# Kernel optimization log

Measured on AMD Instinct MI355X. Metric: run time of the kernel, lower is better.

Reference implementation:

```python
import jax, jax.numpy as jnp
import numpy as np

C = 256        # channels per FPN level (in_channels == representation_size)
PATCH = 5      # GNN kernel_size == stride
NEG_SLOPE = 0.2
K = 7          # node_connectivities[0]


def _conv1x1(x, w, b):
    return jnp.einsum('bchw,oc->bohw', x, w) + b[None, :, None, None]


def _conv3x3(x, w, b):
    y = jax.lax.conv_general_dilated(x, w, (1, 1), 'SAME',
                                     dimension_numbers=('NCHW', 'OIHW', 'NCHW'))
    return y + b[None, :, None, None]


def _nearest(x, hout, wout):
    hin, win = x.shape[-2:]
    ih = (jnp.arange(hout) * hin) // hout
    iw = (jnp.arange(wout) * win) // wout
    return x[..., ih, :][..., iw]


def _topk_edges(score, k, n):
    # torch: A.scatter(1, topk_idx, topk_val); edge = nonzero(triu(A)); edge=[col,row]
    vals, idx = jax.lax.top_k(score, k)          # per-row top-k
    row = jnp.repeat(jnp.arange(n), k)
    col = idx.reshape(-1)
    val = vals.reshape(-1)
    # triu keeps col>=row; GATv2Conv removes self loops then re-adds one per node
    mask = (col > row) & (val != 0.0)
    loop = jnp.arange(n)
    src = jnp.concatenate([col, loop])           # PyG edge_index[0] = source
    dst = jnp.concatenate([row, loop])
    emask = jnp.concatenate([mask, jnp.ones((n,), bool)])
    return src, dst, emask


def _gatv2(x, src, dst, emask, wl, bl, wr, br, att, bias, n):
    heads, dout = att.shape
    xl = (x @ wl + bl).reshape(n, heads, dout)   # source transform (lin_l)
    xr = (x @ wr + br).reshape(n, heads, dout)   # target transform (lin_r)
    m = xl[src] + xr[dst]                        # [E, H, D]
    e = jnp.sum(jax.nn.leaky_relu(m, NEG_SLOPE) * att[None], axis=-1)  # [E, H]
    e = jnp.where(emask[:, None], e, -1e30)
    emax = jax.ops.segment_max(e, dst, num_segments=n)
    w = jnp.exp(e - emax[dst]) * emask[:, None]
    denom = jax.ops.segment_sum(w, dst, num_segments=n)
    alpha = w / (denom[dst] + 1e-16)
    out = jax.ops.segment_sum(alpha[..., None] * xl[src], dst, num_segments=n)
    return out.reshape(n, heads * dout) + bias


def _gnn(x, p, k):
    # x: [1, C, H, W], H,W divisible by PATCH
    _, c, hh, ww = x.shape
    nh, nw = hh // PATCH, ww // PATCH
    n = nh * nw
    patches = x[0].reshape(c, nh, PATCH, nw, PATCH).transpose(1, 3, 0, 2, 4)
    patches = patches.reshape(n, c, PATCH, PATCH)
    emb = jax.nn.relu(jnp.einsum('ncij,ocij->no', patches, p['conv1_w']) + p['conv1_b'])
    emb = jax.nn.relu(emb @ p['fc2_w'].T + p['fc2_b'])
    # feature-similarity kNN graph
    src, dst, em = _topk_edges(emb @ emb.T, k, n)
    h = jax.nn.elu(_gatv2(emb, src, dst, em, *p['g1'], n))
    h = jax.nn.elu(_gatv2(h, src, dst, em, *p['g2'], n))
    # spatial kNN graph (k smallest distances; self distance 0 drops out via val!=0)
    ii, jj = jnp.meshgrid(jnp.arange(nh) * PATCH, jnp.arange(nw) * PATCH, indexing='ij')
    centers = jnp.stack([ii.reshape(-1), jj.reshape(-1)], -1).astype(x.dtype)
    dist = jnp.sqrt(jnp.sum((centers[:, None] - centers[None]) ** 2, -1))
    src2, dst2, em2 = _topk_edges(-dist, k, n)
    h2 = jax.nn.elu(_gatv2(emb, src2, dst2, em2, *p['g3'], n))
    h2 = jax.nn.elu(_gatv2(h2, src2, dst2, em2, *p['g4'], n))
    hc = jax.nn.relu(jnp.concatenate([h, h2], 1) @ p['fc3_w'].T + p['fc3_b']) + h2
    # torch: reshape(dim,dim,C).swapdims(-1,0) -> [C, nw, nh]
    grid = jnp.transpose(hc.reshape(nh, nw, c), (2, 1, 0))
    # ConvTranspose2d(C, C, 5, stride=5): non-overlapping tiling
    up = jnp.einsum('cij,coab->oiajb', grid, p['convT_w'])
    up = up.reshape(c, nw * PATCH, nh * PATCH) + p['convT_b'][:, None, None]
    return jax.nn.relu(up)[None]


def _forward(feat0, feat1, inner_w, inner_b, layer_w, layer_b, convT_w, convT_b,
             conv1_w, conv1_b, fc2_w, fc2_b, fc3_w, fc3_b,
             g1_wl, g1_bl, g1_wr, g1_br, g1_att, g1_bias,
             g2_wl, g2_bl, g2_wr, g2_br, g2_att, g2_bias,
             g3_wl, g3_bl, g3_wr, g3_br, g3_att, g3_bias,
             g4_wl, g4_bl, g4_wr, g4_br, g4_att, g4_bias, k):
    feats = [feat0, feat1]
    xs = []
    for i, f in enumerate(feats):
        p = dict(conv1_w=conv1_w[i], conv1_b=conv1_b[i],
                 fc2_w=fc2_w[i], fc2_b=fc2_b[i],
                 fc3_w=fc3_w[i], fc3_b=fc3_b[i],
                 convT_w=convT_w[i], convT_b=convT_b[i],
                 g1=(g1_wl[i], g1_bl[i], g1_wr[i], g1_br[i], g1_att[i], g1_bias[i]),
                 g2=(g2_wl[i], g2_bl[i], g2_wr[i], g2_br[i], g2_att[i], g2_bias[i]),
                 g3=(g3_wl[i], g3_bl[i], g3_wr[i], g3_br[i], g3_att[i], g3_bias[i]),
                 g4=(g4_wl[i], g4_bl[i], g4_wr[i], g4_br[i], g4_att[i], g4_bias[i]))
        xs.append(f + _gnn(f, p, k))
    # top-down FPN
    last = _conv1x1(xs[1], inner_w[1], inner_b[1])
    out1 = _conv3x3(last, layer_w[1], layer_b[1])
    inner0 = _conv1x1(xs[0], inner_w[0], inner_b[0])
    td = _nearest(last, xs[0].shape[-2], xs[0].shape[-1])
    out0 = _conv3x3(inner0 + td, layer_w[0], layer_b[0])
    return out0, out1


def setup_inputs() -> dict:
    key = jax.random.key(0)
    keys = jax.random.split(key, 48)
    it = iter(range(48))
    def rn(shape, s=0.05):
        return (jax.random.normal(keys[next(it)], shape) * s).astype(jnp.float32)
    H8 = 8 * C
    inp = dict(
        feat0=rn((1, C, 200, 200), 1.0),
        feat1=rn((1, C, 100, 100), 1.0),
        inner_w=rn((2, C, C)), inner_b=rn((2, C)),
        layer_w=rn((2, C, C, 3, 3)), layer_b=rn((2, C)),
        convT_w=rn((2, C, C, PATCH, PATCH)), convT_b=rn((2, C)),
        conv1_w=rn((2, C, C, PATCH, PATCH)), conv1_b=rn((2, C)),
        fc2_w=rn((2, C, C)), fc2_b=rn((2, C)),
        fc3_w=rn((2, C, 2 * C)), fc3_b=rn((2, C)),
        g1_wl=rn((2, C, H8)), g1_bl=rn((2, H8)), g1_wr=rn((2, C, H8)), g1_br=rn((2, H8)),
        g1_att=rn((2, 8, C)), g1_bias=rn((2, H8)),
        g2_wl=rn((2, H8, C)), g2_bl=rn((2, C)), g2_wr=rn((2, H8, C)), g2_br=rn((2, C)),
        g2_att=rn((2, 1, C)), g2_bias=rn((2, C)),
        g3_wl=rn((2, C, H8)), g3_bl=rn((2, H8)), g3_wr=rn((2, C, H8)), g3_br=rn((2, H8)),
        g3_att=rn((2, 8, C)), g3_bias=rn((2, H8)),
        g4_wl=rn((2, H8, C)), g4_bl=rn((2, C)), g4_wr=rn((2, H8, C)), g4_br=rn((2, C)),
        g4_att=rn((2, 1, C)), g4_bias=rn((2, C)),
        k=K,
    )
    return inp


def reference(feat0, feat1, inner_w, inner_b, layer_w, layer_b, convT_w, convT_b,
              conv1_w, conv1_b, fc2_w, fc2_b, fc3_w, fc3_b,
              g1_wl, g1_bl, g1_wr, g1_br, g1_att, g1_bias,
              g2_wl, g2_bl, g2_wr, g2_br, g2_att, g2_bias,
              g3_wl, g3_bl, g3_wr, g3_br, g3_att, g3_bias,
              g4_wl, g4_bl, g4_wr, g4_br, g4_att, g4_bias, k):
    return _forward(feat0, feat1, inner_w, inner_b, layer_w, layer_b, convT_w, convT_b,
                    conv1_w, conv1_b, fc2_w, fc2_b, fc3_w, fc3_b,
                    g1_wl, g1_bl, g1_wr, g1_br, g1_att, g1_bias,
                    g2_wl, g2_bl, g2_wr, g2_br, g2_att, g2_bias,
                    g3_wl, g3_bl, g3_wr, g3_br, g3_att, g3_bias,
                    g4_wl, g4_bl, g4_wr, g4_br, g4_att, g4_bias, k)
```

## Files before the change

### kernel.cpp

```cpp
#include <hip/hip_runtime.h>
#include <cstdint>
#include <cstddef>
#include <math.h>

#define KNN 7

using short8  = __attribute__((ext_vector_type(8))) short;
using floatx4 = __attribute__((ext_vector_type(4))) float;

static const size_t OFF_ARENA = 0;
static const size_t OFF_XS0   = 10240000;
static const size_t OFF_XS1   = 20480000;
static const size_t OFF_LAST  = 23040000;
static const size_t OFF_EMB   = 25600000;
static const size_t OFF_EMB2  = 26009600;
static const size_t OFF_XL    = 26419200;
static const size_t OFF_H1    = 32972800;
static const size_t OFF_XL2   = 36249600;
static const size_t OFF_CAT   = 37068800;
static const size_t OFF_HC    = 37888000;
static const size_t OFF_SRCF  = 38400000;
static const size_t OFF_SRCS  = 38411200;
static const size_t OFF_BF_A  = 38422400;
static const size_t OFF_BF_W  = 40122400;

static __device__ __forceinline__ unsigned short f2bf(float f) {
    union { float f; unsigned u; } v; v.f = f;
    unsigned u = v.u;
    unsigned r = u + 0x7fffu + ((u >> 16) & 1u);
    return (unsigned short)(r >> 16);
}

static __device__ __forceinline__ void glds16(const void* g, void* l) {
    __builtin_amdgcn_global_load_lds((const __attribute__((address_space(1))) void*)g,
                                     (__attribute__((address_space(3))) void*)l, 16, 0, 0);
}

template<int ACT, bool BIAS>
__global__ __launch_bounds__(256)
void gemm_k(const float* __restrict__ A, const float* __restrict__ B,
            const float* __restrict__ bias, float* __restrict__ C, int M, int N, int K)
{
    __shared__ float As[16][68];
    __shared__ float Bs[16][68];
    const int tid = threadIdx.x;
    const int bm0 = blockIdx.y * 64;
    const int bn0 = blockIdx.x * 64;
    const int tx = tid & 15, ty = tid >> 4;
    const int lrow = tid >> 2;
    const int lk4  = (tid & 3) << 2;
    const int m = bm0 + lrow;
    const int nn = bn0 + lrow;
    const bool aok = m < M, bok = nn < N;
    float acc[4][4] = {{0.f,0.f,0.f,0.f},{0.f,0.f,0.f,0.f},{0.f,0.f,0.f,0.f},{0.f,0.f,0.f,0.f}};

    float4 va = {0.f,0.f,0.f,0.f}, vb = {0.f,0.f,0.f,0.f};
    if (aok) va = *(const float4*)(A + (size_t)m * K + lk4);
    if (bok) vb = *(const float4*)(B + (size_t)nn * K + lk4);

    for (int k0 = 0; k0 < K; k0 += 16) {
        As[lk4+0][lrow]=va.x; As[lk4+1][lrow]=va.y; As[lk4+2][lrow]=va.z; As[lk4+3][lrow]=va.w;
        Bs[lk4+0][lrow]=vb.x; Bs[lk4+1][lrow]=vb.y; Bs[lk4+2][lrow]=vb.z; Bs[lk4+3][lrow]=vb.w;
        __syncthreads();
        float4 na = {0.f,0.f,0.f,0.f}, nb = {0.f,0.f,0.f,0.f};
        const bool more = (k0 + 16) < K;
        if (more) {
            if (aok) na = *(const float4*)(A + (size_t)m * K + (k0 + 16 + lk4));
            if (bok) nb = *(const float4*)(B + (size_t)nn * K + (k0 + 16 + lk4));
        }
        #pragma unroll
        for (int k = 0; k < 16; k++) {
            const float4 av = *(const float4*)&As[k][ty << 2];
            const float4 bv = *(const float4*)&Bs[k][tx << 2];
            const float a0=av.x,a1=av.y,a2=av.z,a3=av.w;
            const float b0=bv.x,b1=bv.y,b2=bv.z,b3=bv.w;
            acc[0][0]=fmaf(a0,b0,acc[0][0]); acc[0][1]=fmaf(a0,b1,acc[0][1]);
            acc[0][2]=fmaf(a0,b2,acc[0][2]); acc[0][3]=fmaf(a0,b3,acc[0][3]);
            acc[1][0]=fmaf(a1,b0,acc[1][0]); acc[1][1]=fmaf(a1,b1,acc[1][1]);
            acc[1][2]=fmaf(a1,b2,acc[1][2]); acc[1][3]=fmaf(a1,b3,acc[1][3]);
            acc[2][0]=fmaf(a2,b0,acc[2][0]); acc[2][1]=fmaf(a2,b1,acc[2][1]);
            acc[2][2]=fmaf(a2,b2,acc[2][2]); acc[2][3]=fmaf(a2,b3,acc[2][3]);
            acc[3][0]=fmaf(a3,b0,acc[3][0]); acc[3][1]=fmaf(a3,b1,acc[3][1]);
            acc[3][2]=fmaf(a3,b2,acc[3][2]); acc[3][3]=fmaf(a3,b3,acc[3][3]);
        }
        __syncthreads();
        va = na; vb = nb;
    }
    #pragma unroll
    for (int i = 0; i < 4; i++) {
        const int mm = bm0 + (ty << 2) + i;
        if (mm >= M) continue;
        #pragma unroll
        for (int jj = 0; jj < 4; jj++) {
            const int nc = bn0 + (tx << 2) + jj;
            if (nc >= N) continue;
            float v = acc[i][jj];
            if (BIAS) v += bias[nc];
            if (ACT == 1) v = fmaxf(v, 0.f);
            C[(size_t)mm * N + nc] = v;
        }
    }
}

template<int ACT, bool BIAS>
static inline void gemm32(hipStream_t s, const float* A, const float* B, const float* bias,
                          float* C, int M, int N, int K)
{
    dim3 g((N + 63) / 64, (M + 63) / 64);
    gemm_k<ACT, BIAS><<<g, dim3(256), 0, s>>>(A, B, bias, C, M, N, K);
}

__global__ __launch_bounds__(256)
void gemm32_sk_k(const float* __restrict__ A, const float* __restrict__ B,
                 float* __restrict__ part, int M, int N, int K, int Kc)
{
    __shared__ float As[16][68];
    __shared__ float Bs[16][68];
    const int tid = threadIdx.x;
    const int bm0 = blockIdx.y * 64;
    const int bn0 = blockIdx.x * 64;
    const int sblk = blockIdx.z;
    const int kbeg = sblk * Kc;
    const int kend = (kbeg + Kc < K) ? kbeg + Kc : K;
    const int tx = tid & 15, ty = tid >> 4;
    const int lrow = tid >> 2;
    const int lk4  = (tid & 3) << 2;
    const int m = bm0 + lrow;
    const int nn = bn0 + lrow;
    const bool aok = m < M, bok = nn < N;
    float acc[4][4] = {{0.f,0.f,0.f,0.f},{0.f,0.f,0.f,0.f},{0.f,0.f,0.f,0.f},{0.f,0.f,0.f,0.f}};

    float4 va = {0.f,0.f,0.f,0.f}, vb = {0.f,0.f,0.f,0.f};
    if (aok) va = *(const float4*)(A + (size_t)m * K + kbeg + lk4);
    if (bok) vb = *(const float4*)(B + (size_t)nn * K + kbeg + lk4);

    for (int k0 = kbeg; k0 < kend; k0 += 16) {
        As[lk4+0][lrow]=va.x; As[lk4+1][lrow]=va.y; As[lk4+2][lrow]=va.z; As[lk4+3][lrow]=va.w;
        Bs[lk4+0][lrow]=vb.x; Bs[lk4+1][lrow]=vb.y; Bs[lk4+2][lrow]=vb.z; Bs[lk4+3][lrow]=vb.w;
        __syncthreads();
        float4 na = {0.f,0.f,0.f,0.f}, nb = {0.f,0.f,0.f,0.f};
        const bool more = (k0 + 16) < kend;
        if (more) {
            if (aok) na = *(const float4*)(A + (size_t)m * K + (k0 + 16 + lk4));
            if (bok) nb = *(const float4*)(B + (size_t)nn * K + (k0 + 16 + lk4));
        }
        #pragma unroll
        for (int k = 0; k < 16; k++) {
            const float4 av = *(const float4*)&As[k][ty << 2];
            const float4 bv = *(const float4*)&Bs[k][tx << 2];
            const float a0=av.x,a1=av.y,a2=av.z,a3=av.w;
            const float b0=bv.x,b1=bv.y,b2=bv.z,b3=bv.w;
            acc[0][0]=fmaf(a0,b0,acc[0][0]); acc[0][1]=fmaf(a0,b1,acc[0][1]);
            acc[0][2]=fmaf(a0,b2,acc[0][2]); acc[0][3]=fmaf(a0,b3,acc[0][3]);
            acc[1][0]=fmaf(a1,b0,acc[1][0]); acc[1][1]=fmaf(a1,b1,acc[1][1]);
            acc[1][2]=fmaf(a1,b2,acc[1][2]); acc[1][3]=fmaf(a1,b3,acc[1][3]);
            acc[2][0]=fmaf(a2,b0,acc[2][0]); acc[2][1]=fmaf(a2,b1,acc[2][1]);
            acc[2][2]=fmaf(a2,b2,acc[2][2]); acc[2][3]=fmaf(a2,b3,acc[2][3]);
            acc[3][0]=fmaf(a3,b0,acc[3][0]); acc[3][1]=fmaf(a3,b1,acc[3][1]);
            acc[3][2]=fmaf(a3,b2,acc[3][2]); acc[3][3]=fmaf(a3,b3,acc[3][3]);
        }
        __syncthreads();
        va = na; vb = nb;
    }
    float* P = part + (size_t)sblk * M * N;
    #pragma unroll
    for (int i = 0; i < 4; i++) {
        const int mm = bm0 + (ty << 2) + i;
        if (mm >= M) continue;
        #pragma unroll
        for (int jj = 0; jj < 4; jj++) {
            const int nc = bn0 + (tx << 2) + jj;
            if (nc >= N) continue;
            P[(size_t)mm * N + nc] = acc[i][jj];
        }
    }
}

template<int ACT, bool BIAS>
__global__ void sk_reduce_k(const float* __restrict__ part, const float* __restrict__ bias,
                            float* __restrict__ C, int MN, int N, int S)
{
    const int i4 = (blockIdx.x * 256 + threadIdx.x) * 4;
    if (i4 >= MN) return;
    float4 a = *(const float4*)(part + i4);
    for (int s = 1; s < S; s++) {
        const float4 b = *(const float4*)(part + (size_t)s * MN + i4);
        a.x += b.x; a.y += b.y; a.z += b.z; a.w += b.w;
    }
    if (BIAS) {
        const int n = i4 % N;
        a.x += bias[n]; a.y += bias[n + 1]; a.z += bias[n + 2]; a.w += bias[n + 3];
    }
    if (ACT == 1) {
        a.x = fmaxf(a.x, 0.f); a.y = fmaxf(a.y, 0.f);
        a.z = fmaxf(a.z, 0.f); a.w = fmaxf(a.w, 0.f);
    }
    *(float4*)(C + i4) = a;
}

template<int ACT, bool BIAS>
static inline void gemm32_sk(hipStream_t s, const float* A, const float* B, const float* bias,
                             float* C, float* part, int M, int N, int K, int S)
{
    const int Kc = ((K / S + 15) / 16) * 16;
    dim3 g((N + 63) / 64, (M + 63) / 64, S);
    gemm32_sk_k<<<g, dim3(256), 0, s>>>(A, B, part, M, N, K, Kc);
    const int MN = M * N;
    sk_reduce_k<ACT, BIAS><<<dim3((MN / 4 + 255) / 256), dim3(256), 0, s>>>(part, bias, C, MN, N, S);
}

enum { BT_NT = 0, BT_CONV2 = 2 };


template<int BT, int ACT, int BAX, bool ADDMAT>
__global__ __launch_bounds__(256)
void bgemm_k(const unsigned short* __restrict__ A, const unsigned short* __restrict__ B,
             const float* __restrict__ bias, const float* __restrict__ bias2, int nsplit,
             const float* __restrict__ Dmat, int Dld,
             float* __restrict__ C, int M, int N, int K, int imH, int imW)
{
    __shared__ unsigned short As[2][4096];
    __shared__ unsigned short Bs[2][4096];
    const int tid  = threadIdx.x;
    const int lane = tid & 63;
    const int wid  = tid >> 6;
    const int quad = lane >> 4;
    const int l15  = lane & 15;
    const int wy = wid >> 1, wx = wid & 1;

    int bxx = blockIdx.x, byy = blockIdx.y;
    if (BT == BT_CONV2) {
        const int nbx = gridDim.x;
        const int nwg = nbx * 2;
        const int hw  = byy * nbx + bxx;
        const int q = nwg >> 3, r = nwg & 7;
        const int x8 = hw & 7, d = hw >> 3;
        const int lg = (x8 < r) ? x8 * (q + 1) + d : r * (q + 1) + (x8 - r) * q + d;
        byy = lg & 1; bxx = lg >> 1;
    }
    const int bm0 = byy * 128;
    const int bn0 = bxx * 128;

    floatx4 zero = {0.f, 0.f, 0.f, 0.f};
    floatx4 acc[4][4];
    #pragma unroll
    for (int i = 0; i < 4; i++)
        #pragma unroll
        for (int j = 0; j < 4; j++) acc[i][j] = zero;

    const int l4 = lane >> 2, sc = lane & 3;
    const int r0 = wid * 32 + l4;
    const int r1 = r0 + 16;
    int am0 = bm0 + r0; if (am0 > M - 1) am0 = M - 1;
    int am1 = bm0 + r1; if (am1 > M - 1) am1 = M - 1;
    const unsigned short* aP0 = A + (size_t)am0 * K + sc * 8;
    const unsigned short* aP1 = A + (size_t)am1 * K + sc * 8;

    const unsigned short* bP0 = A;
    const unsigned short* bP1 = A;
    if (BT == BT_NT) {
        int bn0r = bn0 + r0; if (bn0r > N - 1) bn0r = N - 1;
        int bn1r = bn0 + r1; if (bn1r > N - 1) bn1r = N - 1;
        bP0 = B + (size_t)bn0r * K + sc * 8;
        bP1 = B + (size_t)bn1r * K + sc * 8;
    }

    const int crow  = tid >> 1;
    const int chalf = (tid & 1) << 4;
    int cy = 0, cx = 0;
    if (BT == BT_CONV2) {
        int pp = bn0 + crow; if (pp > N - 1) pp = N - 1;
        cy = pp / imW; cx = pp - cy * imW;
    }

    auto stageA = [&](int buf, int k0) {
        glds16(aP0 + k0, &As[buf][(wid * 2 + 0) * 512]);
        glds16(aP1 + k0, &As[buf][(wid * 2 + 1) * 512]);
    };
    auto stageB = [&](int buf, int k0) {
        glds16(bP0 + k0, &Bs[buf][(wid * 2 + 0) * 512]);
        glds16(bP1 + k0, &Bs[buf][(wid * 2 + 1) * 512]);
    };
    auto ldB_conv = [&](int k0, uint4& q0, uint4& q1) {
        const int jj = k0 >> 8;
        const int j3 = jj / 3;
        const int dy = j3 - 1, dx = jj - j3 * 3 - 1;
        const int c0 = k0 & 255;
        const int yy = cy + dy, xx = cx + dx;
        q0 = (uint4){0, 0, 0, 0}; q1 = (uint4){0, 0, 0, 0};
        if ((unsigned)yy < (unsigned)imH && (unsigned)xx < (unsigned)imW) {
            const uint4* p = (const uint4*)(B + (((size_t)yy * imW + xx) << 8) + c0 + chalf);
            q0 = p[0]; q1 = p[1];
        }
    };
    auto wrB = [&](int buf, const uint4& q0, const uint4& q1) {
        *(uint4*)&Bs[buf][crow * 32 + chalf]     = q0;
        *(uint4*)&Bs[buf][crow * 32 + chalf + 8] = q1;
    };
    auto compute = [&](int buf) {
        short8 af[4], bfr[4];
        #pragma unroll
        for (int i = 0; i < 4; i++)
            af[i] = *(const short8*)&As[buf][(wy * 64 + i * 16 + l15) * 32 + quad * 8];
        #pragma unroll
        for (int j = 0; j < 4; j++)
            bfr[j] = *(const short8*)&Bs[buf][(wx * 64 + j * 16 + l15) * 32 + quad * 8];
        #pragma unroll
        for (int i = 0; i < 4; i++)
            #pragma unroll
            for (int j = 0; j < 4; j++)
                acc[i][j] = __builtin_amdgcn_mfma_f32_16x16x32_bf16(af[i], bfr[j], acc[i][j], 0, 0, 0);
    };

    if (BT == BT_NT) {
        stageA(0, 0); stageB(0, 0);
        int bufc = 0;
        for (int k0 = 0; k0 < K; k0 += 32) {
            __syncthreads();
            if (k0 + 32 < K) { stageA(bufc ^ 1, k0 + 32); stageB(bufc ^ 1, k0 + 32); }
            compute(bufc);
            bufc ^= 1;
        }
    } else {
        const int T = K >> 5;
        uint4 r0a, r0b, r1a, r1b, r2a, r2b;
        ldB_conv(0,  r0a, r0b);
        ldB_conv(32, r1a, r1b);
        ldB_conv(64, r2a, r2b);
        stageA(0, 0);
        wrB(0, r0a, r0b);
        auto body = [&](int t, uint4& ca, uint4& cb, uint4& la, uint4& lb) {
            __syncthreads();
            if (t + 3 < T) ldB_conv((t + 3) << 5, la, lb);
            if (t + 1 < T) {
                stageA((t + 1) & 1, (t + 1) << 5);
                wrB((t + 1) & 1, ca, cb);
            }
            compute(t & 1);
        };
        for (int t = 0; t < T; t += 3) {
            body(t,     r1a, r1b, r0a, r0b);
            body(t + 1, r2a, r2b, r1a, r1b);
            body(t + 2, r0a, r0b, r2a, r2b);
        }
    }

    #pragma unroll
    for (int i = 0; i < 4; i++) {
        #pragma unroll
        for (int r = 0; r < 4; r++) {
            const int m = bm0 + wy * 64 + i * 16 + quad * 4 + r;
            if (m >= M) continue;
            #pragma unroll
            for (int j = 0; j < 4; j++) {
                const int n = bn0 + wx * 64 + j * 16 + l15;
                if (n >= N) continue;
                float v = acc[i][j][r];
                if (bias != nullptr)
                    v += (BAX == 0) ? bias[m] : (n < nsplit ? bias[n] : bias2[n - nsplit]);
                if (ACT == 1) v = fmaxf(v, 0.f);
                if (ADDMAT) v += Dmat[(size_t)m * Dld + n];
                C[(size_t)m * N + n] = v;
            }
        }
    }
}

template<int BT, int ACT, int BAX, bool ADDMAT>
static inline void bgemm(hipStream_t s, const unsigned short* A, const unsigned short* B,
                         const float* bias, const float* bias2, int nsplit,
                         const float* D, int Dld, float* C,
                         int M, int N, int K, int imH = 0, int imW = 0)
{
    dim3 g((N + 127) / 128, (M + 127) / 128);
    bgemm_k<BT, ACT, BAX, ADDMAT><<<g, dim3(256), 0, s>>>(A, B, bias, bias2, nsplit,
                                                          D, Dld, C, M, N, K, imH, imW);
}

__global__ __launch_bounds__(256)
void bgemm_sk_k(const unsigned short* __restrict__ A, const unsigned short* __restrict__ B,
                float* __restrict__ part, int M, int N, int K, int Kc)
{
    __shared__ unsigned short As[2][4096];
    __shared__ unsigned short Bs[2][4096];
    const int tid  = threadIdx.x;
    const int lane = tid & 63;
    const int wid  = tid >> 6;
    const int quad = lane >> 4;
    const int l15  = lane & 15;
    const int wy = wid >> 1, wx = wid & 1;
    const int bm0 = blockIdx.y * 128;
    const int bn0 = blockIdx.x * 128;
    const int kbeg = blockIdx.z * Kc;
    const int kend = (kbeg + Kc < K) ? kbeg + Kc : K;

    floatx4 zero = {0.f, 0.f, 0.f, 0.f};
    floatx4 acc[4][4];
    #pragma unroll
    for (int i = 0; i < 4; i++)
        #pragma unroll
        for (int j = 0; j < 4; j++) acc[i][j] = zero;

    const int l4 = lane >> 2, sc = lane & 3;
    const int r0 = wid * 32 + l4;
    const int r1 = r0 + 16;
    int am0 = bm0 + r0; if (am0 > M - 1) am0 = M - 1;
    int am1 = bm0 + r1; if (am1 > M - 1) am1 = M - 1;
    int bn0r = bn0 + r0; if (bn0r > N - 1) bn0r = N - 1;
    int bn1r = bn0 + r1; if (bn1r > N - 1) bn1r = N - 1;
    const unsigned short* aP0 = A + (size_t)am0 * K + sc * 8;
    const unsigned short* aP1 = A + (size_t)am1 * K + sc * 8;
    const unsigned short* bP0 = B + (size_t)bn0r * K + sc * 8;
    const unsigned short* bP1 = B + (size_t)bn1r * K + sc * 8;

    auto stageA = [&](int buf, int k0) {
        glds16(aP0 + k0, &As[buf][(wid * 2 + 0) * 512]);
        glds16(aP1 + k0, &As[buf][(wid * 2 + 1) * 512]);
    };
    auto stageB = [&](int buf, int k0) {
        glds16(bP0 + k0, &Bs[buf][(wid * 2 + 0) * 512]);
        glds16(bP1 + k0, &Bs[buf][(wid * 2 + 1) * 512]);
    };
    auto compute = [&](int buf) {
        short8 af[4], bfr[4];
        #pragma unroll
        for (int i = 0; i < 4; i++)
            af[i] = *(const short8*)&As[buf][(wy * 64 + i * 16 + l15) * 32 + quad * 8];
        #pragma unroll
        for (int j = 0; j < 4; j++)
            bfr[j] = *(const short8*)&Bs[buf][(wx * 64 + j * 16 + l15) * 32 + quad * 8];
        #pragma unroll
        for (int i = 0; i < 4; i++)
            #pragma unroll
            for (int j = 0; j < 4; j++)
                acc[i][j] = __builtin_amdgcn_mfma_f32_16x16x32_bf16(af[i], bfr[j], acc[i][j], 0, 0, 0);
    };

    stageA(0, kbeg); stageB(0, kbeg);
    int bufc = 0;
    for (int k0 = kbeg; k0 < kend; k0 += 32) {
        __syncthreads();
        if (k0 + 32 < kend) { stageA(bufc ^ 1, k0 + 32); stageB(bufc ^ 1, k0 + 32); }
        compute(bufc);
        bufc ^= 1;
    }

    float* P = part + (size_t)blockIdx.z * M * N;
    #pragma unroll
    for (int i = 0; i < 4; i++) {
        #pragma unroll
        for (int r = 0; r < 4; r++) {
            const int m = bm0 + wy * 64 + i * 16 + quad * 4 + r;
            if (m >= M) continue;
            #pragma unroll
            for (int j = 0; j < 4; j++) {
                const int n = bn0 + wx * 64 + j * 16 + l15;
                if (n >= N) continue;
                P[(size_t)m * N + n] = acc[i][j][r];
            }
        }
    }
}

template<int ACT, bool ADDMAT>
__global__ void bsk_reduce_k(const float* __restrict__ part,
                             const float* __restrict__ bias, const float* __restrict__ bias2,
                             int nsplit, const float* __restrict__ Dmat, int Dld,
                             float* __restrict__ C, int MN, int N, int S)
{
    const int i4 = (blockIdx.x * 256 + threadIdx.x) * 4;
    if (i4 >= MN) return;
    float4 a = *(const float4*)(part + i4);
    for (int s = 1; s < S; s++) {
        const float4 b = *(const float4*)(part + (size_t)s * MN + i4);
        a.x += b.x; a.y += b.y; a.z += b.z; a.w += b.w;
    }
    const int n = i4 % N;
    const float* bb = (n < nsplit) ? (bias + n) : (bias2 + n - nsplit);
    a.x += bb[0]; a.y += bb[1]; a.z += bb[2]; a.w += bb[3];
    if (ACT == 1) {
        a.x = fmaxf(a.x, 0.f); a.y = fmaxf(a.y, 0.f);
        a.z = fmaxf(a.z, 0.f); a.w = fmaxf(a.w, 0.f);
    }
    if (ADDMAT) {
        const int m = i4 / N;
        const float4 d = *(const float4*)(Dmat + (size_t)m * Dld + n);
        a.x += d.x; a.y += d.y; a.z += d.z; a.w += d.w;
    }
    *(float4*)(C + i4) = a;
}

template<int ACT, bool ADDMAT>
static inline void bgemm_sk(hipStream_t s, const unsigned short* A, const unsigned short* B,
                            const float* bias, const float* bias2, int nsplit,
                            const float* D, int Dld, float* C, float* part,
                            int M, int N, int K, int S)
{
    const int Kc = ((K / S + 31) / 32) * 32;
    dim3 g((N + 127) / 128, (M + 127) / 128, S);
    bgemm_sk_k<<<g, dim3(256), 0, s>>>(A, B, part, M, N, K, Kc);
    const int MN = M * N;
    bsk_reduce_k<ACT, ADDMAT><<<dim3((MN / 4 + 255) / 256), dim3(256), 0, s>>>(
        part, bias, bias2, nsplit, D, Dld, C, MN, N, S);
}

__global__ void cast_bf16_k(const float* __restrict__ in, unsigned short* __restrict__ out, int total)
{
    const int i4 = (blockIdx.x * 256 + threadIdx.x) * 4;
    if (i4 + 4 <= total) {
        const float4 v = *(const float4*)(in + i4);
        ushort4 o;
        o.x = f2bf(v.x); o.y = f2bf(v.y); o.z = f2bf(v.z); o.w = f2bf(v.w);
        *(ushort4*)(out + i4) = o;
    } else {
        for (int i = i4; i < total; i++) out[i] = f2bf(in[i]);
    }
}

static inline void cast_bf(hipStream_t s, const float* in, unsigned short* out, int total)
{
    cast_bf16_k<<<dim3((total / 4 + 255) / 256), dim3(256), 0, s>>>(in, out, total);
}

__device__ __forceinline__ void cast_t_body(const float* __restrict__ in,
                                            unsigned short* __restrict__ out, int K, int N)
{
    __shared__ float tile[64][65];
    const int n0 = blockIdx.x * 64;
    const int k0 = blockIdx.y * 64;
    const int t = threadIdx.x;
    const int r = t >> 2;
    const int c4 = (t & 3) << 4;
    {
        const int k = k0 + r;
        if (k < K && n0 + c4 + 16 <= N) {
            const float4* p = (const float4*)(in + (size_t)k * N + n0 + c4);
            *(float4*)&tile[r][c4]      = p[0];
            *(float4*)&tile[r][c4 + 4]  = p[1];
            *(float4*)&tile[r][c4 + 8]  = p[2];
            *(float4*)&tile[r][c4 + 12] = p[3];
        } else {
            for (int i = 0; i < 16; i++)
                tile[r][c4 + i] = (k < K && n0 + c4 + i < N) ? in[(size_t)k * N + n0 + c4 + i] : 0.f;
        }
    }
    __syncthreads();
    const int n = n0 + r;
    if (n >= N) return;
    unsigned short tmp[16];
    #pragma unroll
    for (int i = 0; i < 16; i++) tmp[i] = f2bf(tile[c4 + i][r]);
    if (k0 + 64 <= K) {
        *(uint4*)(out + (size_t)n * K + k0 + c4)     = *(uint4*)&tmp[0];
        *(uint4*)(out + (size_t)n * K + k0 + c4 + 8) = *(uint4*)&tmp[8];
    } else {
        for (int i = 0; i < 16; i++)
            if (k0 + c4 + i < K) out[(size_t)n * K + k0 + c4 + i] = tmp[i];
    }
}

__global__ void cast_t_k(const float* __restrict__ in, unsigned short* __restrict__ out, int K, int N)
{
    cast_t_body(in, out, K, N);
}

__global__ void cast_t2_k(const float* __restrict__ in0, const float* __restrict__ in1,
                          unsigned short* __restrict__ out0, unsigned short* __restrict__ out1,
                          int K, int N)
{
    if (blockIdx.z == 0) cast_t_body(in0, out0, K, N);
    else                 cast_t_body(in1, out1, K, N);
}

static inline void cast_t(hipStream_t s, const float* in, unsigned short* out, int K, int N)
{
    cast_t_k<<<dim3((N + 63) / 64, (K + 63) / 64), dim3(256), 0, s>>>(in, out, K, N);
}

static inline void cast_t2(hipStream_t s, const float* in0, const float* in1,
                           unsigned short* out0, unsigned short* out1, int K, int N)
{
    cast_t2_k<<<dim3((N + 63) / 64, (K + 63) / 64, 2), dim3(256), 0, s>>>(in0, in1, out0, out1, K, N);
}

__global__ void reorder_w3_k(const float* __restrict__ in, unsigned short* __restrict__ out)
{
    const int idx = blockIdx.x * 256 + threadIdx.x;
    if (idx >= 589824) return;
    const int o = idx / 2304;
    const int r = idx - o * 2304;
    const int j = r >> 8;
    const int c = r & 255;
    out[idx] = f2bf(in[(size_t)o * 2304 + c * 9 + j]);
}

__global__ void extract_patches_k(const float* __restrict__ f, float* __restrict__ patches,
                                  int nw, int H, int total)
{
    int idx = blockIdx.x * 256 + threadIdx.x;
    if (idx >= total) return;
    int q = idx % 6400;
    int p = idx / 6400;
    int c = q / 25;
    int rem = q - c * 25;
    int a = rem / 5, b = rem - (rem / 5) * 5;
    int ih = p / nw, iw = p - (p / nw) * nw;
    patches[idx] = f[(size_t)c * H * H + (size_t)(ih * 5 + a) * H + (iw * 5 + b)];
}

__global__ void topk_feat_k(const float* __restrict__ score, int* __restrict__ srcCols, int n)
{
    const int r = blockIdx.x;
    const int lane = threadIdx.x;
    const float* row = score + (size_t)r * n;
    int   sel[KNN];
    float selv[KNN];
    #pragma unroll
    for (int t = 0; t < KNN; t++) {
        float best = -__builtin_huge_valf();
        int   bidx = 0x7fffffff;
        for (int c = lane; c < n; c += 64) {
            bool taken = false;
            #pragma unroll
            for (int u = 0; u < KNN; u++)
                if (u < t && sel[u] == c) taken = true;
            if (taken) continue;
            float v = row[c];
            if (v > best || (v == best && c < bidx)) { best = v; bidx = c; }
        }
        #pragma unroll
        for (int off = 32; off > 0; off >>= 1) {
            float ov = __shfl_down(best, off);
            int   oi = __shfl_down(bidx, off);
            if (ov > best || (ov == best && oi < bidx)) { best = ov; bidx = oi; }
        }
        best = __shfl(best, 0);
        bidx = __shfl(bidx, 0);
        sel[t] = bidx; selv[t] = best;
    }
    if (lane < KNN) {
        int c = -1; float v = 0.f;
        #pragma unroll
        for (int t = 0; t < KNN; t++)
            if (lane == t) { c = sel[t]; v = selv[t]; }
        srcCols[r * KNN + lane] = (c > r && v != 0.0f) ? c : -1;
    }
}

__global__ void topk_spatial_k(int* __restrict__ srcCols, int n, int nw)
{
    const int r = blockIdx.x;
    const int lane = threadIdx.x;
    const int ri = r / nw, rj = r - (r / nw) * nw;
    int sel[KNN];
    #pragma unroll
    for (int t = 0; t < KNN; t++) {
        int bkey = 0x7fffffff;
        for (int c = lane; c < n; c += 64) {
            bool taken = false;
            #pragma unroll
            for (int u = 0; u < KNN; u++)
                if (u < t && sel[u] == c) taken = true;
            if (taken) continue;
            const int ci = c / nw, cj = c - (c / nw) * nw;
            const int dy = (ri - ci) * 5, dx = (rj - cj) * 5;
            const int d2 = dy * dy + dx * dx;
            const int key = (d2 << 11) | c;
            if (key < bkey) bkey = key;
        }
        #pragma unroll
        for (int off = 32; off > 0; off >>= 1) {
            int ok = __shfl_down(bkey, off);
            if (ok < bkey) bkey = ok;
        }
        bkey = __shfl(bkey, 0);
        sel[t] = bkey & 2047;
    }
    if (lane < KNN) {
        int c = -1;
        #pragma unroll
        for (int t = 0; t < KNN; t++) if (lane == t) c = sel[t];
        srcCols[r * KNN + lane] = (c > r) ? c : -1;
    }
}

__global__ void gat_fused_k(const float* __restrict__ x, int xroff, int xstride,
                            const float* __restrict__ att,
                            const int* __restrict__ srcCols, const float* __restrict__ bias,
                            float* __restrict__ out, int n, int H, int ostride, int ooff)
{
    const int wid = (blockIdx.x * blockDim.x + threadIdx.x) >> 6;
    const int lane = threadIdx.x & 63;
    if (wid >= n * H) return;
    const int h = wid % H;
    const int r = wid / H;
    const int d0 = lane << 2;

    const float4 xrf  = *(const float4*)(x + (size_t)r * xstride + xroff + h * 256 + d0);
    const float4 attf = *(const float4*)(att + (size_t)h * 256 + d0);

    int srcs[8];
    #pragma unroll
    for (int s_ = 0; s_ < KNN; s_++) srcs[s_] = srcCols[r * KNN + s_];
    srcs[7] = r;

    float4 xlf[8];
    float  e[8];
    #pragma unroll
    for (int s_ = 0; s_ < 8; s_++) {
        const int c = srcs[s_];
        float4 v = {0.f, 0.f, 0.f, 0.f};
        if (c >= 0) v = *(const float4*)(x + (size_t)c * xstride + h * 256 + d0);
        xlf[s_] = v;
        float m, p = 0.f;
        m = v.x + xrf.x; m = (m > 0.f) ? m : 0.2f * m; p += m * attf.x;
        m = v.y + xrf.y; m = (m > 0.f) ? m : 0.2f * m; p += m * attf.y;
        m = v.z + xrf.z; m = (m > 0.f) ? m : 0.2f * m; p += m * attf.z;
        m = v.w + xrf.w; m = (m > 0.f) ? m : 0.2f * m; p += m * attf.w;
        #pragma unroll
        for (int off = 32; off > 0; off >>= 1) p += __shfl_down(p, off);
        e[s_] = __shfl(p, 0);
    }

    float mx = e[7];
    #pragma unroll
    for (int s_ = 0; s_ < KNN; s_++)
        if (srcs[s_] >= 0) mx = fmaxf(mx, e[s_]);
    float a[8], denom = 0.f;
    #pragma unroll
    for (int s_ = 0; s_ < 8; s_++) {
        a[s_] = (s_ == 7 || srcs[s_] >= 0) ? expf(e[s_] - mx) : 0.f;
        denom += a[s_];
    }
    const float inv = 1.f / (denom + 1e-16f);

    float o0 = 0.f, o1 = 0.f, o2 = 0.f, o3 = 0.f;
    #pragma unroll
    for (int s_ = 0; s_ < 8; s_++) {
        const float al = a[s_] * inv;
        o0 = fmaf(al, xlf[s_].x, o0); o1 = fmaf(al, xlf[s_].y, o1);
        o2 = fmaf(al, xlf[s_].z, o2); o3 = fmaf(al, xlf[s_].w, o3);
    }
    const float* bb = bias + (size_t)h * 256 + d0;
    o0 += bb[0]; o1 += bb[1]; o2 += bb[2]; o3 += bb[3];
    o0 = (o0 > 0.f) ? o0 : (expf(o0) - 1.f);
    o1 = (o1 > 0.f) ? o1 : (expf(o1) - 1.f);
    o2 = (o2 > 0.f) ? o2 : (expf(o2) - 1.f);
    o3 = (o3 > 0.f) ? o3 : (expf(o3) - 1.f);
    float4 res = {o0, o1, o2, o3};
    *(float4*)(out + (size_t)r * ostride + ooff + (size_t)h * 256 + d0) = res;
}

__global__ void scatter_convT_k(const float* __restrict__ f, const float* __restrict__ U,
                                const float* __restrict__ bias, float* __restrict__ xs,
                                int nw, int H, int total)
{
    int idx = blockIdx.x * 256 + threadIdx.x;
    if (idx >= total) return;
    int x = idx % H;
    int t = idx / H;
    int y = t % H;
    int o = t / H;
    int j = y / 5, a = y - j * 5;
    int i = x / 5, b = x - i * 5;
    int p = i * nw + j;
    float v = U[(size_t)p * 6400 + o * 25 + a * 5 + b] + bias[o];
    v = fmaxf(v, 0.f);
    xs[idx] = f[idx] + v;
}

__global__ void upsample_add_k(float* __restrict__ acc, const float* __restrict__ last,
                               int H, int Hs, int total)
{
    int idx = blockIdx.x * 256 + threadIdx.x;
    if (idx >= total) return;
    int x = idx % H;
    int t = idx / H;
    int y = t % H;
    int c = t / H;
    acc[idx] += last[(size_t)c * Hs * Hs + (size_t)(y >> 1) * Hs + (x >> 1)];
}

static void run_level(void* const* d_in, float* ws, int l, int H, hipStream_t s)
{
    const float* f = (const float*)d_in[l];
    const int nh = H / 5, nw = nh, n = nh * nw, HW = H * H;

    const float* convT_w = (const float*)d_in[6]  + (size_t)l * 1638400;
    const float* convT_b = (const float*)d_in[7]  + l * 256;
    const float* conv1_w = (const float*)d_in[8]  + (size_t)l * 1638400;
    const float* conv1_b = (const float*)d_in[9]  + l * 256;
    const float* fc2_w   = (const float*)d_in[10] + (size_t)l * 65536;
    const float* fc2_b   = (const float*)d_in[11] + l * 256;
    const float* fc3_w   = (const float*)d_in[12] + (size_t)l * 131072;
    const float* fc3_b   = (const float*)d_in[13] + l * 256;
    const float* g1_wl   = (const float*)d_in[14] + (size_t)l * 524288;
    const float* g1_bl   = (const float*)d_in[15] + l * 2048;
    const float* g1_wr   = (const float*)d_in[16] + (size_t)l * 524288;
    const float* g1_br   = (const float*)d_in[17] + l * 2048;
    const float* g1_att  = (const float*)d_in[18] + l * 2048;
    const float* g1_bias = (const float*)d_in[19] + l * 2048;
    const float* g2_wl   = (const float*)d_in[20] + (size_t)l * 524288;
    const float* g2_bl   = (const float*)d_in[21] + l * 256;
    const float* g2_wr   = (const float*)d_in[22] + (size_t)l * 524288;
    const float* g2_br   = (const float*)d_in[23] + l * 256;
    const float* g2_att  = (const float*)d_in[24] + l * 256;
    const float* g2_bias = (const float*)d_in[25] + l * 256;
    const float* g3_wl   = (const float*)d_in[26] + (size_t)l * 524288;
    const float* g3_bl   = (const float*)d_in[27] + l * 2048;
    const float* g3_wr   = (const float*)d_in[28] + (size_t)l * 524288;
    const float* g3_br   = (const float*)d_in[29] + l * 2048;
    const float* g3_att  = (const float*)d_in[30] + l * 2048;
    const float* g3_bias = (const float*)d_in[31] + l * 2048;
    const float* g4_wl   = (const float*)d_in[32] + (size_t)l * 524288;
    const float* g4_bl   = (const float*)d_in[33] + l * 256;
    const float* g4_wr   = (const float*)d_in[34] + (size_t)l * 524288;
    const float* g4_br   = (const float*)d_in[35] + l * 256;
    const float* g4_att  = (const float*)d_in[36] + l * 256;
    const float* g4_bias = (const float*)d_in[37] + l * 256;

    float* patches = ws + OFF_ARENA;
    float* xs    = ws + (l == 0 ? OFF_XS0 : OFF_XS1);
    float* emb   = ws + OFF_EMB;
    float* emb2  = ws + OFF_EMB2;
    float* score = ws + OFF_LAST;
    float* xlr   = ws + OFF_XL;
    float* h1    = ws + OFF_H1;
    float* xlr2  = ws + OFF_XL2;
    float* cat   = ws + OFF_CAT;
    float* hc    = ws + OFF_HC;
    int* srcF = (int*)(ws + OFF_SRCF);
    int* srcS = (int*)(ws + OFF_SRCS);
    unsigned short* ba = (unsigned short*)(ws + OFF_BF_A);
    unsigned short* bw = (unsigned short*)(ws + OFF_BF_W);
    float* part = ws + OFF_ARENA;

    { int tot = n * 6400;
      extract_patches_k<<<dim3((tot + 255) / 256), dim3(256), 0, s>>>(f, patches, nw, H, tot); }

    gemm32_sk<1, true>(s, patches, conv1_w, conv1_b, emb, xlr, n, 256, 6400, 16);
    gemm32<1, true>(s, emb, fc2_w, fc2_b, emb2, n, 256, 256);
    gemm32<0, false>(s, emb2, emb2, nullptr, score, n, n, 256);
    topk_feat_k<<<dim3(n), dim3(64), 0, s>>>(score, srcF, n);
    topk_spatial_k<<<dim3(n), dim3(64), 0, s>>>(srcS, n, nw);

    const int gatw1 = n * 8;
    const int gatw2 = n;

    cast_bf(s, emb2, ba, n * 256);
    cast_t2(s, g1_wl, g1_wr, bw, bw + 2048 * 256, 256, 2048);
    if (n >= 1024)
        bgemm<BT_NT, 0, 1, false>(s, ba, bw, g1_bl, g1_br, 2048, nullptr, 0, xlr, n, 4096, 256);
    else
        bgemm_sk<0, false>(s, ba, bw, g1_bl, g1_br, 2048, nullptr, 0, xlr, part, n, 4096, 256, 2);
    gat_fused_k<<<dim3((gatw1 + 3) / 4), dim3(256), 0, s>>>(xlr, 2048, 4096, g1_att, srcF, g1_bias, h1, n, 8, 2048, 0);

    cast_bf(s, h1, ba, n * 2048);
    cast_t2(s, g2_wl, g2_wr, bw, bw + 256 * 2048, 2048, 256);
    bgemm_sk<0, false>(s, ba, bw, g2_bl, g2_br, 256, nullptr, 0, xlr2, part, n, 512, 2048, 8);
    gat_fused_k<<<dim3((gatw2 + 3) / 4), dim3(256), 0, s>>>(xlr2, 256, 512, g2_att, srcF, g2_bias, cat, n, 1, 512, 0);

    cast_bf(s, emb2, ba, n * 256);
    cast_t2(s, g3_wl, g3_wr, bw, bw + 2048 * 256, 256, 2048);
    if (n >= 1024)
        bgemm<BT_NT, 0, 1, false>(s, ba, bw, g3_bl, g3_br, 2048, nullptr, 0, xlr, n, 4096, 256);
    else
        bgemm_sk<0, false>(s, ba, bw, g3_bl, g3_br, 2048, nullptr, 0, xlr, part, n, 4096, 256, 2);
    gat_fused_k<<<dim3((gatw1 + 3) / 4), dim3(256), 0, s>>>(xlr, 2048, 4096, g3_att, srcS, g3_bias, h1, n, 8, 2048, 0);

    cast_bf(s, h1, ba, n * 2048);
    cast_t2(s, g4_wl, g4_wr, bw, bw + 256 * 2048, 2048, 256);
    bgemm_sk<0, false>(s, ba, bw, g4_bl, g4_br, 256, nullptr, 0, xlr2, part, n, 512, 2048, 8);
    gat_fused_k<<<dim3((gatw2 + 3) / 4), dim3(256), 0, s>>>(xlr2, 256, 512, g4_att, srcS, g4_bias, cat, n, 1, 512, 256);

    cast_bf(s, cat, ba, n * 512);
    cast_bf(s, fc3_w, bw, 131072);
    bgemm_sk<1, true>(s, ba, bw, fc3_b, fc3_b, 256, cat + 256, 512, hc, part, n, 256, 512, 4);
    cast_bf(s, hc, ba, n * 256);
    cast_t(s, convT_w, bw, 256, 6400);
    bgemm<BT_NT, 0, 1, false>(s, ba, bw, nullptr, nullptr, 0, nullptr, 0, patches, n, 6400, 256);
    { int tot = 256 * HW;
      scatter_convT_k<<<dim3((tot + 255) / 256), dim3(256), 0, s>>>(f, patches, convT_b, xs, nw, H, tot); }
}

extern "C" void kernel_launch(void* const* d_in, const int* in_sizes, int n_in,
                              void* d_out, int out_size, void* d_ws, size_t ws_size,
                              hipStream_t stream)
{
    float* ws  = (float*)d_ws;
    float* out = (float*)d_out;

    run_level(d_in, ws, 0, 200, stream);
    run_level(d_in, ws, 1, 100, stream);

    const float* inner_w = (const float*)d_in[2];
    const float* inner_b = (const float*)d_in[3];
    const float* layer_w = (const float*)d_in[4];
    const float* layer_b = (const float*)d_in[5];
    float* xs0    = ws + OFF_XS0;
    float* xs1    = ws + OFF_XS1;
    float* last   = ws + OFF_LAST;
    float* inner0 = ws + OFF_ARENA;
    unsigned short* bimg = (unsigned short*)(ws + OFF_XL);
    unsigned short* bw1  = (unsigned short*)(ws + OFF_BF_W);
    unsigned short* bwc  = (unsigned short*)(ws + OFF_BF_W + 100000);

    cast_t(stream, xs1, bimg, 256, 10000);
    cast_bf(stream, inner_w + 65536, bw1, 65536);
    bgemm<BT_NT, 0, 0, false>(stream, bw1, bimg, inner_b + 256, nullptr, 0, nullptr, 0,
                              last, 256, 10000, 256);
    reorder_w3_k<<<dim3((589824 + 255) / 256), dim3(256), 0, stream>>>(layer_w + 589824, bwc);
    cast_t(stream, last, bimg, 256, 10000);
    bgemm<BT_CONV2, 0, 0, false>(stream, bwc, bimg, layer_b + 256, nullptr, 0, nullptr, 0,
                                 out + 10240000, 256, 10000, 2304, 100, 100);

    cast_t(stream, xs0, bimg, 256, 40000);
    cast_bf(stream, inner_w, bw1, 65536);
    bgemm<BT_NT, 0, 0, false>(stream, bw1, bimg, inner_b, nullptr, 0, nullptr, 0,
                              inner0, 256, 40000, 256);
    { int tot = 256 * 40000;
      upsample_add_k<<<dim3((tot + 255) / 256), dim3(256), 0, stream>>>(inner0, last, 200, 100, tot); }
    reorder_w3_k<<<dim3((589824 + 255) / 256), dim3(256), 0, stream>>>(layer_w, bwc);
    cast_t(stream, inner0, bimg, 256, 40000);
    bgemm<BT_CONV2, 0, 0, false>(stream, bwc, bimg, layer_b, nullptr, 0, nullptr, 0,
                                 out, 256, 40000, 2304, 200, 200);
}
```

Baseline: 1.209 ms.

## Triple-buffer bf16 GEMMs, swizzle LDS, and zero-pad conv input for direct loads

The bf16 MFMA GEMM kernels move from double to triple-buffered LDS staging, using explicit vmcnt waits and raw barriers so two tiles are in flight while one is computed. LDS rows are XOR-swizzled on both the global-to-LDS writes and the fragment reads to cut bank conflicts. The 3x3 conv input is now written into a zero-padded (H+2)x(W+2) NHWC bf16 buffer with a separate ring-zeroing kernel, so the conv B operand uses the same direct global-to-LDS loads as the plain GEMM instead of bounds-checked register loads followed by LDS writes. This raises LDS use per block, which may lower occupancy, and the tile-swizzle remap is now selected by gridDim.y==2 rather than by template type.

After: 1.156 ms. -4.4%, faster.

```diff
diff --git a/kernel.cpp b/kernel.cpp
--- a/kernel.cpp
+++ b/kernel.cpp
@@ -211,7 +211,6 @@
 
 enum { BT_NT = 0, BT_CONV2 = 2 };
 
-
 template<int BT, int ACT, int BAX, bool ADDMAT>
 __global__ __launch_bounds__(256)
 void bgemm_k(const unsigned short* __restrict__ A, const unsigned short* __restrict__ B,
@@ -219,8 +218,8 @@
              const float* __restrict__ Dmat, int Dld,
              float* __restrict__ C, int M, int N, int K, int imH, int imW)
 {
-    __shared__ unsigned short As[2][4096];
-    __shared__ unsigned short Bs[2][4096];
+    __shared__ unsigned short As[3][4096];
+    __shared__ unsigned short Bs[3][4096];
     const int tid  = threadIdx.x;
     const int lane = tid & 63;
     const int wid  = tid >> 6;
@@ -229,7 +228,7 @@
     const int wy = wid >> 1, wx = wid & 1;
 
     int bxx = blockIdx.x, byy = blockIdx.y;
-    if (BT == BT_CONV2) {
+    if (gridDim.y == 2) {
         const int nbx = gridDim.x;
         const int nwg = nbx * 2;
         const int hw  = byy * nbx + bxx;
@@ -248,63 +247,57 @@
         #pragma unroll
         for (int j = 0; j < 4; j++) acc[i][j] = zero;
 
-    const int l4 = lane >> 2, sc = lane & 3;
+    const int l4 = lane >> 2;
+    const int swc = (((lane & 3) ^ ((lane >> 3) & 3)) << 3);
     const int r0 = wid * 32 + l4;
     const int r1 = r0 + 16;
     int am0 = bm0 + r0; if (am0 > M - 1) am0 = M - 1;
     int am1 = bm0 + r1; if (am1 > M - 1) am1 = M - 1;
-    const unsigned short* aP0 = A + (size_t)am0 * K + sc * 8;
-    const unsigned short* aP1 = A + (size_t)am1 * K + sc * 8;
-
-    const unsigned short* bP0 = A;
-    const unsigned short* bP1 = A;
+    const unsigned short* aP0 = A + (size_t)am0 * K + swc;
+    const unsigned short* aP1 = A + (size_t)am1 * K + swc;
+
+    const unsigned short* bP0;
+    const unsigned short* bP1;
     if (BT == BT_NT) {
         int bn0r = bn0 + r0; if (bn0r > N - 1) bn0r = N - 1;
         int bn1r = bn0 + r1; if (bn1r > N - 1) bn1r = N - 1;
-        bP0 = B + (size_t)bn0r * K + sc * 8;
-        bP1 = B + (size_t)bn1r * K + sc * 8;
-    }
-
-    const int crow  = tid >> 1;
-    const int chalf = (tid & 1) << 4;
-    int cy = 0, cx = 0;
-    if (BT == BT_CONV2) {
-        int pp = bn0 + crow; if (pp > N - 1) pp = N - 1;
-        cy = pp / imW; cx = pp - cy * imW;
-    }
-
-    auto stageA = [&](int buf, int k0) {
-        glds16(aP0 + k0, &As[buf][(wid * 2 + 0) * 512]);
-        glds16(aP1 + k0, &As[buf][(wid * 2 + 1) * 512]);
+        bP0 = B + (size_t)bn0r * K + swc;
+        bP1 = B + (size_t)bn1r * K + swc;
+    } else {
+        const int W2 = imW + 2;
+        int pp0 = bn0 + r0; if (pp0 > N - 1) pp0 = N - 1;
+        int pp1 = bn0 + r1; if (pp1 > N - 1) pp1 = N - 1;
+        const int py0 = pp0 / imW, px0 = pp0 - py0 * imW;
+        const int py1 = pp1 / imW, px1 = pp1 - py1 * imW;
+        bP0 = B + ((size_t)(py0 + 1) * W2 + px0 + 1) * 256 + swc;
+        bP1 = B + ((size_t)(py1 + 1) * W2 + px1 + 1) * 256 + swc;
+    }
+
+    auto stage = [&](int buf, int t) {
+        const int k0 = t << 5;
+        glds16(aP0 + k0, &As[buf][wid * 1024]);
+        glds16(aP1 + k0, &As[buf][wid * 1024 + 512]);
+        if (BT == BT_NT) {
+            glds16(bP0 + k0, &Bs[buf][wid * 1024]);
+            glds16(bP1 + k0, &Bs[buf][wid * 1024 + 512]);
+        } else {
+            const int jj = k0 >> 8;
+            const int j3 = jj / 3;
+            const ptrdiff_t toff = (ptrdiff_t)((j3 - 1) * (imW + 2) + (jj - j3 * 3 - 1)) * 256
+                                 + (k0 & 255);
+            glds16(bP0 + toff, &Bs[buf][wid * 1024]);
+            glds16(bP1 + toff, &Bs[buf][wid * 1024 + 512]);
+        }
     };
-    auto stageB = [&](int buf, int k0) {
-        glds16(bP0 + k0, &Bs[buf][(wid * 2 + 0) * 512]);
-        glds16(bP1 + k0, &Bs[buf][(wid * 2 + 1) * 512]);
-    };
-    auto ldB_conv = [&](int k0, uint4& q0, uint4& q1) {
-        const int jj = k0 >> 8;
-        const int j3 = jj / 3;
-        const int dy = j3 - 1, dx = jj - j3 * 3 - 1;
-        const int c0 = k0 & 255;
-        const int yy = cy + dy, xx = cx + dx;
-        q0 = (uint4){0, 0, 0, 0}; q1 = (uint4){0, 0, 0, 0};
-        if ((unsigned)yy < (unsigned)imH && (unsigned)xx < (unsigned)imW) {
-            const uint4* p = (const uint4*)(B + (((size_t)yy * imW + xx) << 8) + c0 + chalf);
-            q0 = p[0]; q1 = p[1];
-        }
-    };
-    auto wrB = [&](int buf, const uint4& q0, const uint4& q1) {
-        *(uint4*)&Bs[buf][crow * 32 + chalf]     = q0;
-        *(uint4*)&Bs[buf][crow * 32 + chalf + 8] = q1;
-    };
+    const int rsw = ((quad ^ ((l15 >> 1) & 3)) << 3);
     auto compute = [&](int buf) {
         short8 af[4], bfr[4];
         #pragma unroll
         for (int i = 0; i < 4; i++)
-            af[i] = *(const short8*)&As[buf][(wy * 64 + i * 16 + l15) * 32 + quad * 8];
+            af[i] = *(const short8*)&As[buf][(wy * 64 + i * 16 + l15) * 32 + rsw];
         #pragma unroll
         for (int j = 0; j < 4; j++)
-            bfr[j] = *(const short8*)&Bs[buf][(wx * 64 + j * 16 + l15) * 32 + quad * 8];
+            bfr[j] = *(const short8*)&Bs[buf][(wx * 64 + j * 16 + l15) * 32 + rsw];
         #pragma unroll
         for (int i = 0; i < 4; i++)
             #pragma unroll
@@ -312,37 +305,19 @@
                 acc[i][j] = __builtin_amdgcn_mfma_f32_16x16x32_bf16(af[i], bfr[j], acc[i][j], 0, 0, 0);
     };
 
-    if (BT == BT_NT) {
-        stageA(0, 0); stageB(0, 0);
-        int bufc = 0;
-        for (int k0 = 0; k0 < K; k0 += 32) {
-            __syncthreads();
-            if (k0 + 32 < K) { stageA(bufc ^ 1, k0 + 32); stageB(bufc ^ 1, k0 + 32); }
-            compute(bufc);
-            bufc ^= 1;
-        }
-    } else {
-        const int T = K >> 5;
-        uint4 r0a, r0b, r1a, r1b, r2a, r2b;
-        ldB_conv(0,  r0a, r0b);
-        ldB_conv(32, r1a, r1b);
-        ldB_conv(64, r2a, r2b);
-        stageA(0, 0);
-        wrB(0, r0a, r0b);
-        auto body = [&](int t, uint4& ca, uint4& cb, uint4& la, uint4& lb) {
-            __syncthreads();
-            if (t + 3 < T) ldB_conv((t + 3) << 5, la, lb);
-            if (t + 1 < T) {
-                stageA((t + 1) & 1, (t + 1) << 5);
-                wrB((t + 1) & 1, ca, cb);
-            }
-            compute(t & 1);
-        };
-        for (int t = 0; t < T; t += 3) {
-            body(t,     r1a, r1b, r0a, r0b);
-            body(t + 1, r2a, r2b, r1a, r1b);
-            body(t + 2, r0a, r0b, r2a, r2b);
-        }
+    const int T = K >> 5;
+    stage(0, 0);
+    if (T > 1) stage(1, 1);
+    int cb = 0, sb = 2;
+    for (int t = 0; t < T; t++) {
+        if (t < T - 1) asm volatile("s_waitcnt vmcnt(4) lgkmcnt(0)" ::: "memory");
+        else           asm volatile("s_waitcnt vmcnt(0) lgkmcnt(0)" ::: "memory");
+        __builtin_amdgcn_s_barrier();
+        __builtin_amdgcn_sched_barrier(0);
+        if (t + 2 < T) stage(sb, t + 2);
+        compute(cb);
+        cb = (cb == 2) ? 0 : cb + 1;
+        sb = (sb == 2) ? 0 : sb + 1;
     }
 
     #pragma unroll
@@ -381,8 +356,8 @@
 void bgemm_sk_k(const unsigned short* __restrict__ A, const unsigned short* __restrict__ B,
                 float* __restrict__ part, int M, int N, int K, int Kc)
 {
-    __shared__ unsigned short As[2][4096];
-    __shared__ unsigned short Bs[2][4096];
+    __shared__ unsigned short As[3][4096];
+    __shared__ unsigned short Bs[3][4096];
     const int tid  = threadIdx.x;
     const int lane = tid & 63;
     const int wid  = tid >> 6;
@@ -401,34 +376,35 @@
         #pragma unroll
         for (int j = 0; j < 4; j++) acc[i][j] = zero;
 
-    const int l4 = lane >> 2, sc = lane & 3;
+    const int l4 = lane >> 2;
+    const int swc = (((lane & 3) ^ ((lane >> 3) & 3)) << 3);
     const int r0 = wid * 32 + l4;
     const int r1 = r0 + 16;
     int am0 = bm0 + r0; if (am0 > M - 1) am0 = M - 1;
     int am1 = bm0 + r1; if (am1 > M - 1) am1 = M - 1;
     int bn0r = bn0 + r0; if (bn0r > N - 1) bn0r = N - 1;
     int bn1r = bn0 + r1; if (bn1r > N - 1) bn1r = N - 1;
-    const unsigned short* aP0 = A + (size_t)am0 * K + sc * 8;
-    const unsigned short* aP1 = A + (size_t)am1 * K + sc * 8;
-    const unsigned short* bP0 = B + (size_t)bn0r * K + sc * 8;
-    const unsigned short* bP1 = B + (size_t)bn1r * K + sc * 8;
-
-    auto stageA = [&](int buf, int k0) {
-        glds16(aP0 + k0, &As[buf][(wid * 2 + 0) * 512]);
-        glds16(aP1 + k0, &As[buf][(wid * 2 + 1) * 512]);
+    const unsigned short* aP0 = A + (size_t)am0 * K + kbeg + swc;
+    const unsigned short* aP1 = A + (size_t)am1 * K + kbeg + swc;
+    const unsigned short* bP0 = B + (size_t)bn0r * K + kbeg + swc;
+    const unsigned short* bP1 = B + (size_t)bn1r * K + kbeg + swc;
+
+    auto stage = [&](int buf, int t) {
+        const int k0 = t << 5;
+        glds16(aP0 + k0, &As[buf][wid * 1024]);
+        glds16(aP1 + k0, &As[buf][wid * 1024 + 512]);
+        glds16(bP0 + k0, &Bs[buf][wid * 1024]);
+        glds16(bP1 + k0, &Bs[buf][wid * 1024 + 512]);
     };
-    auto stageB = [&](int buf, int k0) {
-        glds16(bP0 + k0, &Bs[buf][(wid * 2 + 0) * 512]);
-        glds16(bP1 + k0, &Bs[buf][(wid * 2 + 1) * 512]);
-    };
+    const int rsw = ((quad ^ ((l15 >> 1) & 3)) << 3);
     auto compute = [&](int buf) {
         short8 af[4], bfr[4];
         #pragma unroll
         for (int i = 0; i < 4; i++)
-            af[i] = *(const short8*)&As[buf][(wy * 64 + i * 16 + l15) * 32 + quad * 8];
+            af[i] = *(const short8*)&As[buf][(wy * 64 + i * 16 + l15) * 32 + rsw];
         #pragma unroll
         for (int j = 0; j < 4; j++)
-            bfr[j] = *(const short8*)&Bs[buf][(wx * 64 + j * 16 + l15) * 32 + quad * 8];
+            bfr[j] = *(const short8*)&Bs[buf][(wx * 64 + j * 16 + l15) * 32 + rsw];
         #pragma unroll
         for (int i = 0; i < 4; i++)
             #pragma unroll
@@ -436,13 +412,19 @@
                 acc[i][j] = __builtin_amdgcn_mfma_f32_16x16x32_bf16(af[i], bfr[j], acc[i][j], 0, 0, 0);
     };
 
-    stageA(0, kbeg); stageB(0, kbeg);
-    int bufc = 0;
-    for (int k0 = kbeg; k0 < kend; k0 += 32) {
-        __syncthreads();
-        if (k0 + 32 < kend) { stageA(bufc ^ 1, k0 + 32); stageB(bufc ^ 1, k0 + 32); }
-        compute(bufc);
-        bufc ^= 1;
+    const int T = (kend - kbeg) >> 5;
+    stage(0, 0);
+    if (T > 1) stage(1, 1);
+    int cb = 0, sb = 2;
+    for (int t = 0; t < T; t++) {
+        if (t < T - 1) asm volatile("s_waitcnt vmcnt(4) lgkmcnt(0)" ::: "memory");
+        else           asm volatile("s_waitcnt vmcnt(0) lgkmcnt(0)" ::: "memory");
+        __builtin_amdgcn_s_barrier();
+        __builtin_amdgcn_sched_barrier(0);
+        if (t + 2 < T) stage(sb, t + 2);
+        compute(cb);
+        cb = (cb == 2) ? 0 : cb + 1;
+        sb = (sb == 2) ? 0 : sb + 1;
     }
 
     float* P = part + (size_t)blockIdx.z * M * N;
@@ -581,6 +563,67 @@
                            unsigned short* out0, unsigned short* out1, int K, int N)
 {
     cast_t2_k<<<dim3((N + 63) / 64, (K + 63) / 64, 2), dim3(256), 0, s>>>(in0, in1, out0, out1, K, N);
+}
+
+__global__ void cast_t_pad_k(const float* __restrict__ in, unsigned short* __restrict__ out,
+                             int N, int imW)
+{
+    __shared__ float tile[64][65];
+    const int n0 = blockIdx.x * 64;
+    const int k0 = blockIdx.y * 64;
+    const int t = threadIdx.x;
+    const int r = t >> 2;
+    const int c4 = (t & 3) << 4;
+    {
+        const int k = k0 + r;
+        if (n0 + c4 + 16 <= N) {
+            const float4* p = (const float4*)(in + (size_t)k * N + n0 + c4);
+            *(float4*)&tile[r][c4]      = p[0];
+            *(float4*)&tile[r][c4 + 4]  = p[1];
+            *(float4*)&tile[r][c4 + 8]  = p[2];
+            *(float4*)&tile[r][c4 + 12] = p[3];
+        } else {
+            for (int i = 0; i < 16; i++)
+                tile[r][c4 + i] = (n0 + c4 + i < N) ? in[(size_t)k * N + n0 + c4 + i] : 0.f;
+        }
+    }
+    __syncthreads();
+    const int n = n0 + r;
+    if (n >= N) return;
+    const int py = n / imW, px = n - py * imW;
+    unsigned short tmp[16];
+    #pragma unroll
+    for (int i = 0; i < 16; i++) tmp[i] = f2bf(tile[c4 + i][r]);
+    unsigned short* o = out + ((size_t)(py + 1) * (imW + 2) + px + 1) * 256 + k0 + c4;
+    *(uint4*)(o)     = *(uint4*)&tmp[0];
+    *(uint4*)(o + 8) = *(uint4*)&tmp[8];
+}
+
+static inline void cast_t_pad(hipStream_t s, const float* in, unsigned short* out, int N, int imW)
+{
+    cast_t_pad_k<<<dim3((N + 63) / 64, 4), dim3(256), 0, s>>>(in, out, N, imW);
+}
+
+__global__ void zero_ring_k(unsigned short* __restrict__ out, int imH, int imW)
+{
+    const int W2 = imW + 2;
+    const int nb = 2 * W2 + 2 * imH;
+    const int idx = blockIdx.x * 256 + threadIdx.x;
+    if (idx >= nb * 32) return;
+    const int p = idx >> 5;
+    const int c8 = (idx & 31) << 3;
+    int row;
+    if (p < W2)            row = p;
+    else if (p < 2 * W2)   row = (imH + 1) * W2 + (p - W2);
+    else { const int q = p - 2 * W2; const int y = q >> 1;
+           row = (y + 1) * W2 + ((q & 1) ? (imW + 1) : 0); }
+    *(uint4*)(out + (size_t)row * 256 + c8) = (uint4){0, 0, 0, 0};
+}
+
+static inline void zero_ring(hipStream_t s, unsigned short* out, int imH, int imW)
+{
+    const int tot = (2 * (imW + 2) + 2 * imH) * 32;
+    zero_ring_k<<<dim3((tot + 255) / 256), dim3(256), 0, s>>>(out, imH, imW);
 }
 
 __global__ void reorder_w3_k(const float* __restrict__ in, unsigned short* __restrict__ out)
@@ -910,7 +953,8 @@
     bgemm<BT_NT, 0, 0, false>(stream, bw1, bimg, inner_b + 256, nullptr, 0, nullptr, 0,
                               last, 256, 10000, 256);
     reorder_w3_k<<<dim3((589824 + 255) / 256), dim3(256), 0, stream>>>(layer_w + 589824, bwc);
-    cast_t(stream, last, bimg, 256, 10000);
+    zero_ring(stream, bimg, 100, 100);
+    cast_t_pad(stream, last, bimg, 10000, 100);
     bgemm<BT_CONV2, 0, 0, false>(stream, bwc, bimg, layer_b + 256, nullptr, 0, nullptr, 0,
                                  out + 10240000, 256, 10000, 2304, 100, 100);
 
@@ -921,7 +965,8 @@
     { int tot = 256 * 40000;
       upsample_add_k<<<dim3((tot + 255) / 256), dim3(256), 0, stream>>>(inner0, last, 200, 100, tot); }
     reorder_w3_k<<<dim3((589824 + 255) / 256), dim3(256), 0, stream>>>(layer_w, bwc);
-    cast_t(stream, inner0, bimg, 256, 40000);
+    zero_ring(stream, bimg, 200, 200);
+    cast_t_pad(stream, inner0, bimg, 40000, 200);
     bgemm<BT_CONV2, 0, 0, false>(stream, bwc, bimg, layer_b, nullptr, 0, nullptr, 0,
                                  out, 256, 40000, 2304, 200, 200);
 }
```
